# Optimization experiments

Hardware: AMD Instinct MI355X
Metric: run time of the kernel (lower is better)

## Reference

```python
import jax, jax.numpy as jnp
import numpy as np
import math

L, B, D, H = 2048, 4, 1024, 16
DK = D // H
DFF = 4 * D
EPS = 1e-5


def setup_inputs() -> dict:
    key = jax.random.key(0)
    ks = jax.random.split(key, 16)
    s = 1.0 / math.sqrt(D)
    sf = 1.0 / math.sqrt(DFF)
    return {
        "x": jax.random.normal(ks[0], (L, B, D), jnp.float32),
        "Wq": jax.random.normal(ks[1], (D, D), jnp.float32) * s,
        "bq": jnp.zeros((D,), jnp.float32),
        "Wk": jax.random.normal(ks[2], (D, D), jnp.float32) * s,
        "bk": jnp.zeros((D,), jnp.float32),
        "Wv": jax.random.normal(ks[3], (D, D), jnp.float32) * s,
        "bv": jnp.zeros((D,), jnp.float32),
        "Wo": jax.random.normal(ks[4], (D, D), jnp.float32) * s,
        "bo": jnp.zeros((D,), jnp.float32),
        "W1": jax.random.normal(ks[5], (D, DFF), jnp.float32) * s,
        "b1": jnp.zeros((DFF,), jnp.float32),
        "W2": jax.random.normal(ks[6], (DFF, D), jnp.float32) * sf,
        "b2": jnp.zeros((D,), jnp.float32),
        "g1": jnp.ones((D,), jnp.float32),
        "be1": jnp.zeros((D,), jnp.float32),
        "g2": jnp.ones((D,), jnp.float32),
        "be2": jnp.zeros((D,), jnp.float32),
    }


def _layer_norm(x, g, b):
    mu = jnp.mean(x, axis=-1, keepdims=True)
    var = jnp.var(x, axis=-1, keepdims=True)
    return (x - mu) * jax.lax.rsqrt(var + EPS) * g + b


def reference(x, Wq, bq, Wk, bk, Wv, bv, Wo, bo, W1, b1, W2, b2, g1, be1, g2, be2):
    # x: (L, B, D)
    q = x @ Wq + bq
    k = x @ Wk + bk
    v = x @ Wv + bv
    # (L,B,H,dk) -> (B,H,L,dk)
    q = q.reshape(L, B, H, DK).transpose(1, 2, 0, 3)
    k = k.reshape(L, B, H, DK).transpose(1, 2, 0, 3)
    v = v.reshape(L, B, H, DK).transpose(1, 2, 0, 3)
    scale = 1.0 / math.sqrt(DK)
    scores = jnp.einsum('bhqd,bhkd->bhqk', q, k) * scale
    w = jax.nn.softmax(scores, axis=-1)
    attn = jnp.einsum('bhqk,bhkd->bhqd', w, v)  # (B,H,L,dk)
    attn = attn.transpose(2, 0, 1, 3).reshape(L, B, D)
    attn_out = attn @ Wo + bo
    x = _layer_norm(x + attn_out, g1, be1)
    h = jax.nn.gelu(x @ W1 + b1, approximate=False)
    ff = h @ W2 + b2
    return _layer_norm(x + ff, g2, be2)
```

## Files before the change

### kernel.cpp

```cpp
#include <hip/hip_runtime.h>

#define L_   2048
#define B_   4
#define D_   1024
#define H_   16
#define DK_  64
#define DFF_ 4096
#define NT_  (L_*B_)

typedef unsigned short u16;
typedef unsigned int   u32;
typedef __bf16 bf16x8 __attribute__((ext_vector_type(8)));
typedef float  f32x4  __attribute__((ext_vector_type(4)));

__device__ __forceinline__ u16 f2bf(float f) {
  u32 u = __float_as_uint(f);
  u += 0x7fffu + ((u >> 16) & 1u);
  return (u16)(u >> 16);
}
__device__ __forceinline__ float bf2f(u32 lo16) {
  return __uint_as_float(lo16 << 16);
}

#define GLDS16(g, l) __builtin_amdgcn_global_load_lds( \
    (const __attribute__((address_space(1))) void*)(g), \
    (__attribute__((address_space(3))) void*)(l), 16, 0, 0)

#define SCQ_ 0.18033688011112042f

__global__ __launch_bounds__(256) void transpose_w_k(
    const float* __restrict__ W, u16* __restrict__ Wt, int K, int N)
{
  __shared__ float tile[32][33];
  int n0 = blockIdx.x * 32, k0 = blockIdx.y * 32;
  int tx = threadIdx.x, ty = threadIdx.y;
#pragma unroll
  for (int i = ty; i < 32; i += 8)
    tile[i][tx] = W[(size_t)(k0 + i) * N + n0 + tx];
  __syncthreads();
#pragma unroll
  for (int i = ty; i < 32; i += 8)
    Wt[(size_t)(n0 + i) * K + k0 + tx] = f2bf(tile[tx][i]);
}

__global__ __launch_bounds__(256) void transpose_w4_k(
    const float* __restrict__ W0, const float* __restrict__ W1,
    const float* __restrict__ W2, const float* __restrict__ W3,
    u16* __restrict__ dst)
{
  __shared__ float tile[32][33];
  int z = blockIdx.z;
  const float* W = (z == 0) ? W0 : (z == 1) ? W1 : (z == 2) ? W2 : W3;
  u16* Wt = dst + (size_t)z * 1048576;
  int n0 = blockIdx.x * 32, k0 = blockIdx.y * 32;
  int tx = threadIdx.x, ty = threadIdx.y;
#pragma unroll
  for (int i = ty; i < 32; i += 8)
    tile[i][tx] = W[(size_t)(k0 + i) * 1024 + n0 + tx];
  __syncthreads();
#pragma unroll
  for (int i = ty; i < 32; i += 8)
    Wt[(size_t)(n0 + i) * 1024 + k0 + tx] = f2bf(tile[tx][i]);
}

__global__ __launch_bounds__(256) void f32_to_bf16_k(
    const float* __restrict__ in, u16* __restrict__ out, int n4)
{
  int i = blockIdx.x * 256 + threadIdx.x;
  if (i >= n4) return;
  float4 v = ((const float4*)in)[i];
  uint2 r;
  r.x = (u32)f2bf(v.x) | ((u32)f2bf(v.y) << 16);
  r.y = (u32)f2bf(v.z) | ((u32)f2bf(v.w) << 16);
  ((uint2*)out)[i] = r;
}

__global__ __launch_bounds__(256) void bias_concat_k(
    const float* __restrict__ bq, const float* __restrict__ bk,
    const float* __restrict__ bv, float* __restrict__ o)
{
  int i = blockIdx.x * 256 + threadIdx.x;
  float v = (i < 1024) ? bq[i] : ((i < 2048) ? bk[i - 1024] : bv[i - 2048]);
  o[i] = v;
}

template<int EPI>
__global__ __launch_bounds__(512, 2)
void gemm_pipe(const u16* __restrict__ A, const u16* __restrict__ Bt,
               const float* __restrict__ bias, const void* __restrict__ res,
               u16* __restrict__ outb, int M, int N, int K)
{
  constexpr int BM = 256, BN = 128, BK = 64;
  constexpr int ABYTES = BM * BK * 2;
  constexpr int BUFB = (BM + BN) * BK * 2;
  __shared__ char SM[3 * BUFB];

  const int tid = threadIdx.x;
  const int w = tid >> 6, lane = tid & 63;
  const int l15 = lane & 15, l4 = lane >> 4;
  const int NK = K >> 6;

  const int gx = gridDim.x;
  int nwg = gx * gridDim.y;
  int id = blockIdx.y * gx + blockIdx.x;
  int q = nwg >> 3, r = nwg & 7;
  int xcd = id & 7, idx = id >> 3;
  int wg = (xcd < r ? xcd * (q + 1) : r * (q + 1) + (xcd - r) * q) + idx;
  const int m0 = (wg / gx) * BM, n0 = (wg % gx) * BN;
  const int wm = (w >> 1) * 64, wn = (w & 1) * 64;

  const u16* gsrc[6];
#pragma unroll
  for (int u = 0; u < 6; ++u) {
    int o = u * 8192 + tid * 16;
    int row; const u16* base;
    if (o < ABYTES) {
      row = o >> 7;
      base = A + (size_t)(m0 + row) * K;
    } else {
      int ob = o - ABYTES;
      row = ob >> 7;
      base = Bt + (size_t)(n0 + row) * K;
    }
    int col8 = ((o >> 4) & 7) ^ (row & 7);
    gsrc[u] = base + col8 * 8;
  }

  auto stage = [&](int t, int u) {
    const u16* s = gsrc[u] + (size_t)((t < NK) ? t : 0) * BK;
    GLDS16(s, SM + (t % 3) * BUFB + u * 8192 + w * 1024);
  };

  for (int tt = 0; tt < 2; ++tt)
#pragma unroll
    for (int u = 0; u < 6; ++u) stage(tt, u);
  asm volatile("s_waitcnt vmcnt(6)" ::: "memory");
  asm volatile("s_barrier" ::: "memory");

  f32x4 acc[4][4];
#pragma unroll
  for (int i = 0; i < 4; ++i)
#pragma unroll
    for (int j = 0; j < 4; ++j) acc[i][j] = (f32x4){0.f, 0.f, 0.f, 0.f};

  for (int t = 0; t < NK; ++t) {
    const char* rb = SM + (t % 3) * BUFB;
    const int tn = t + 2;
#pragma unroll
    for (int ph = 0; ph < 2; ++ph) {
      bf16x8 af[4], bfr[4];
#pragma unroll
      for (int mi = 0; mi < 4; ++mi) {
        int row = wm + mi * 16 + l15;
        af[mi] = *(const bf16x8*)(rb + row * 128 +
                                  (((ph * 4 + l4) ^ (l15 & 7)) << 4));
      }
      stage(tn, ph * 3 + 0);
#pragma unroll
      for (int nj = 0; nj < 4; ++nj) {
        int row = wn + nj * 16 + l15;
        bfr[nj] = *(const bf16x8*)(rb + ABYTES + row * 128 +
                                   (((ph * 4 + l4) ^ (l15 & 7)) << 4));
      }
      stage(tn, ph * 3 + 1);
      stage(tn, ph * 3 + 2);
      __builtin_amdgcn_s_setprio(1);
#pragma unroll
      for (int mi = 0; mi < 4; ++mi)
#pragma unroll
        for (int nj = 0; nj < 4; ++nj)
          acc[mi][nj] = __builtin_amdgcn_mfma_f32_16x16x32_bf16(
              af[mi], bfr[nj], acc[mi][nj], 0, 0, 0);
      __builtin_amdgcn_s_setprio(0);
    }
    asm volatile("s_waitcnt lgkmcnt(0)" ::: "memory");
    asm volatile("s_waitcnt vmcnt(6)" ::: "memory");
    asm volatile("s_barrier" ::: "memory");
  }
  asm volatile("s_waitcnt vmcnt(0)" ::: "memory");

  const int gm = m0 + wm + l4 * 4;
  const int gn = n0 + wn + l15;
#pragma unroll
  for (int mi = 0; mi < 4; ++mi) {
#pragma unroll
    for (int nj = 0; nj < 4; ++nj) {
      int col = gn + nj * 16;
      float bv = bias[col];
#pragma unroll
      for (int rr = 0; rr < 4; ++rr) {
        int row = gm + mi * 16 + rr;
        float v = acc[mi][nj][rr] + bv;
        if (EPI == 2) {
          float gv = 0.5f * v * (1.f + erff(v * 0.70710678118654752f));
          outb[(size_t)row * N + col] = f2bf(gv);
        } else if (EPI == 3) {
          int which = col >> 10, c1 = col & 1023;
          int ll = row >> 2, bb = row & 3;
          int hh = c1 >> 6, dd = c1 & 63;
          if (which == 0) v *= SCQ_;
          outb[(size_t)which * 8388608 +
               ((((size_t)(bb * H_ + hh)) * L_ + ll) << 6) + dd] = f2bf(v);
        } else if (EPI == 5) {
          size_t idxo = (size_t)row * N + col;
          outb[idxo] = f2bf(v + ((const float*)res)[idxo]);
        } else {
          size_t idxo = (size_t)row * N + col;
          outb[idxo] = f2bf(v + bf2f(((const u16*)res)[idxo]));
        }
      }
    }
  }
}

__global__ __launch_bounds__(256, 3)
void attn_fwd2(const u16* __restrict__ qp, const u16* __restrict__ kp,
               const u16* __restrict__ vp, u16* __restrict__ op)
{
  __shared__ u16 Ks[2][64 * 64];
  __shared__ u16 Vt[2][64 * 64];
  const int tid = threadIdx.x, w = tid >> 6, lane = tid & 63;
  const int l15 = lane & 15, l4 = lane >> 4;
  const int n = blockIdx.x;
  const int bh = (n & 7) | ((n >> 7) << 3);
  const int qi = (n >> 3) & 15;
  const int q0 = qi * 128;
  const u16* qb = qp + (size_t)bh * L_ * DK_;
  const u16* kb = kp + (size_t)bh * L_ * DK_;
  const u16* vb = vp + (size_t)bh * L_ * DK_;

  bf16x8 qf[2][2];
#pragma unroll
  for (int g = 0; g < 2; ++g)
#pragma unroll
    for (int kk = 0; kk < 2; ++kk)
      qf[g][kk] = *(const bf16x8*)&qb[(size_t)(q0 + g * 64 + w * 16 + l15) * DK_ +
                                      kk * 32 + l4 * 8];

  f32x4 accO[2][4];
  f32x4 lacc[2];
#pragma unroll
  for (int g = 0; g < 2; ++g) {
#pragma unroll
    for (int i = 0; i < 4; ++i) accO[g][i] = (f32x4){0.f, 0.f, 0.f, 0.f};
    lacc[g] = (f32x4){0.f, 0.f, 0.f, 0.f};
  }

  bf16x8 oneb;
  {
    u32 ob = (l15 == 0) ? 0x3f803f80u : 0u;
#pragma unroll
    for (int j = 0; j < 4; ++j) ((u32*)&oneb)[j] = ob;
  }

  int rho0 = tid >> 3, rho1 = (256 + tid) >> 3, cseg = lane & 7;
  int kv0 = (rho0 & 32) | ((rho0 & 12) << 1) | ((rho0 & 16) >> 2) | (rho0 & 3);
  int kv1 = (rho1 & 32) | ((rho1 & 12) << 1) | ((rho1 & 16) >> 2) | (rho1 & 3);
  const u16* ksrc0 = kb + (size_t)kv0 * DK_ + ((cseg ^ (rho0 & 7)) << 3);
  const u16* ksrc1 = kb + (size_t)kv1 * DK_ + ((cseg ^ (rho1 & 7)) << 3);

  const int vseg = tid & 7, vkvp = tid >> 3;
  const u16* vsrc = vb + (size_t)(vkvp * 2) * DK_ + vseg * 8;
  u32 voff[8];
#pragma unroll
  for (int dd2 = 0; dd2 < 4; ++dd2) {
    int d0 = vseg * 8 + dd2 * 2, d1 = d0 + 1;
    voff[dd2 * 2] = d0 * 128 +
        ((((vkvp >> 2) ^ (d0 & 7) ^ (d0 >> 3)) << 4) | ((vkvp & 3) << 2));
    voff[dd2 * 2 + 1] = d1 * 128 +
        ((((vkvp >> 2) ^ (d1 & 7) ^ (d1 >> 3)) << 4) | ((vkvp & 3) << 2));
  }

  auto packV = [&](int buf, uint4 a, uint4 b) {
#pragma unroll
    for (int dd2 = 0; dd2 < 4; ++dd2) {
      u32 ai = ((const u32*)&a)[dd2], bi = ((const u32*)&b)[dd2];
      *(u32*)((char*)Vt[buf] + voff[dd2 * 2])     = __builtin_amdgcn_perm(bi, ai, 0x05040100u);
      *(u32*)((char*)Vt[buf] + voff[dd2 * 2 + 1]) = __builtin_amdgcn_perm(bi, ai, 0x07060302u);
    }
  };

  auto exp_pack = [&](f32x4 (&s)[4], u32 (&pk)[2][4]) {
#pragma unroll
    for (int i = 0; i < 4; ++i)
#pragma unroll
      for (int rr = 0; rr < 4; ++rr) s[i][rr] = exp2f(s[i][rr]);
#pragma unroll
    for (int kk = 0; kk < 2; ++kk)
#pragma unroll
      for (int j2 = 0; j2 < 4; ++j2) {
        int nb = kk * 2 + (j2 >> 1);
        int rr = (j2 & 1) * 2;
        u32 rres;
        asm("v_cvt_pk_bf16_f32 %0, %1, %2" : "=v"(rres)
            : "v"(s[nb][rr]), "v"(s[nb][rr + 1]));
        pk[kk][j2] = rres;
      }
  };

  {
    uint4 a = *(const uint4*)vsrc;
    uint4 b = *(const uint4*)(vsrc + DK_);
    GLDS16(ksrc0, &Ks[0][w * 512]);
    GLDS16(ksrc1, &Ks[0][2048 + w * 512]);
    packV(0, a, b);
  }
  __syncthreads();

  constexpr int NTI = L_ / 64;
  for (int t = 0; t < NTI; ++t) {
    const int cur = t & 1;
    const bool pf = (t + 1 < NTI);
    const int tn = pf ? t + 1 : t;

    uint4 va = *(const uint4*)(vsrc + (size_t)(tn * 64) * DK_);
    uint4 vbv = *(const uint4*)(vsrc + (size_t)(tn * 64) * DK_ + DK_);
    if (pf) {
      GLDS16(ksrc0 + (size_t)((t + 1) * 64) * DK_, &Ks[cur ^ 1][w * 512]);
      GLDS16(ksrc1 + (size_t)((t + 1) * 64) * DK_, &Ks[cur ^ 1][2048 + w * 512]);
    }

    f32x4 s0[4], s1[4];
#pragma unroll
    for (int i = 0; i < 4; ++i) {
      s0[i] = (f32x4){0.f, 0.f, 0.f, 0.f};
      s1[i] = (f32x4){0.f, 0.f, 0.f, 0.f};
    }
#pragma unroll
    for (int kk = 0; kk < 2; ++kk) {
#pragma unroll
      for (int nb = 0; nb < 4; ++nb) {
        int row = nb * 16 + l15;
        bf16x8 kf = *(const bf16x8*)((const char*)Ks[cur] + row * 128 +
                                     (((kk * 4 + l4) ^ (row & 7)) << 4));
        s0[nb] = __builtin_amdgcn_mfma_f32_16x16x32_bf16(kf, qf[0][kk], s0[nb], 0, 0, 0);
        s1[nb] = __builtin_amdgcn_mfma_f32_16x16x32_bf16(kf, qf[1][kk], s1[nb], 0, 0, 0);
      }
    }

    u32 pk0[2][4], pk1[2][4];
    exp_pack(s0, pk0);
    exp_pack(s1, pk1);

    if (pf) packV(cur ^ 1, va, vbv);

#pragma unroll
    for (int kk = 0; kk < 2; ++kk) {
      bf16x8 pa0, pa1;
      ((u32*)&pa0)[0] = pk0[kk][0]; ((u32*)&pa0)[1] = pk0[kk][1];
      ((u32*)&pa0)[2] = pk0[kk][2]; ((u32*)&pa0)[3] = pk0[kk][3];
      ((u32*)&pa1)[0] = pk1[kk][0]; ((u32*)&pa1)[1] = pk1[kk][1];
      ((u32*)&pa1)[2] = pk1[kk][2]; ((u32*)&pa1)[3] = pk1[kk][3];
      lacc[0] = __builtin_amdgcn_mfma_f32_16x16x32_bf16(pa0, oneb, lacc[0], 0, 0, 0);
      lacc[1] = __builtin_amdgcn_mfma_f32_16x16x32_bf16(pa1, oneb, lacc[1], 0, 0, 0);
#pragma unroll
      for (int nb2 = 0; nb2 < 4; ++nb2) {
        int drow = nb2 * 16 + l15;
        bf16x8 vf = *(const bf16x8*)((const char*)Vt[cur] + drow * 128 +
                                     (((kk * 4 + l4) ^ (drow & 7) ^ (drow >> 3)) << 4));
        accO[0][nb2] = __builtin_amdgcn_mfma_f32_16x16x32_bf16(pa0, vf, accO[0][nb2], 0, 0, 0);
        accO[1][nb2] = __builtin_amdgcn_mfma_f32_16x16x32_bf16(pa1, vf, accO[1][nb2], 0, 0, 0);
      }
    }
    __syncthreads();
  }

  const int bb = bh >> 4, hh = bh & 15;
#pragma unroll
  for (int g = 0; g < 2; ++g) {
#pragma unroll
    for (int rr = 0; rr < 4; ++rr) {
      float ls = __shfl(lacc[g][rr], l4 << 4);
      float rl = 1.f / ls;
      int qg = q0 + g * 64 + w * 16 + l4 * 4 + rr;
      size_t base = ((size_t)qg * B_ + bb) * D_ + hh * 64;
#pragma unroll
      for (int nb2 = 0; nb2 < 4; ++nb2)
        op[base + nb2 * 16 + l15] = f2bf(accO[g][nb2][rr] * rl);
    }
  }
}

__global__ __launch_bounds__(256) void layernorm_bf_k(
    const u16* __restrict__ y, const float* __restrict__ g, const float* __restrict__ be,
    float* __restrict__ of, u16* __restrict__ ob)
{
  int row = blockIdx.x, tid = threadIdx.x;
  uint2 raw = *(const uint2*)&y[(size_t)row * D_ + tid * 4];
  float v0 = bf2f(raw.x & 0xffffu), v1 = bf2f(raw.x >> 16);
  float v2 = bf2f(raw.y & 0xffffu), v3 = bf2f(raw.y >> 16);
  float s = (v0 + v1) + (v2 + v3);
  float ss = v0 * v0 + v1 * v1 + v2 * v2 + v3 * v3;
#pragma unroll
  for (int msk = 32; msk >= 1; msk >>= 1) {
    s += __shfl_xor(s, msk);
    ss += __shfl_xor(ss, msk);
  }
  __shared__ float rs[4], rss[4];
  if ((tid & 63) == 0) { rs[tid >> 6] = s; rss[tid >> 6] = ss; }
  __syncthreads();
  s = rs[0] + rs[1] + rs[2] + rs[3];
  ss = rss[0] + rss[1] + rss[2] + rss[3];
  float mu = s * (1.f / D_);
  float var = ss * (1.f / D_) - mu * mu;
  float rstd = rsqrtf(var + 1e-5f);
  int c = tid * 4;
  float o0 = (v0 - mu) * rstd * g[c + 0] + be[c + 0];
  float o1 = (v1 - mu) * rstd * g[c + 1] + be[c + 1];
  float o2 = (v2 - mu) * rstd * g[c + 2] + be[c + 2];
  float o3 = (v3 - mu) * rstd * g[c + 3] + be[c + 3];
  if (of) {
    float4 o = {o0, o1, o2, o3};
    *(float4*)&of[(size_t)row * D_ + c] = o;
  }
  if (ob) {
    uint2 r;
    r.x = (u32)f2bf(o0) | ((u32)f2bf(o1) << 16);
    r.y = (u32)f2bf(o2) | ((u32)f2bf(o3) << 16);
    *(uint2*)&ob[(size_t)row * D_ + c] = r;
  }
}

extern "C" void kernel_launch(void* const* d_in, const int* in_sizes, int n_in,
                              void* d_out, int out_size, void* d_ws, size_t ws_size,
                              hipStream_t stream)
{
  const float* x   = (const float*)d_in[0];
  const float* Wq  = (const float*)d_in[1];
  const float* bq  = (const float*)d_in[2];
  const float* Wk  = (const float*)d_in[3];
  const float* bk  = (const float*)d_in[4];
  const float* Wv  = (const float*)d_in[5];
  const float* bv  = (const float*)d_in[6];
  const float* Wo  = (const float*)d_in[7];
  const float* bo  = (const float*)d_in[8];
  const float* W1f = (const float*)d_in[9];
  const float* b1  = (const float*)d_in[10];
  const float* W2f = (const float*)d_in[11];
  const float* b2  = (const float*)d_in[12];
  const float* g1  = (const float*)d_in[13];
  const float* be1 = (const float*)d_in[14];
  const float* g2  = (const float*)d_in[15];
  const float* be2 = (const float*)d_in[16];

  char* ws = (char*)d_ws;
  const size_t MB = 1024 * 1024;
  u16* WqT  = (u16*)(ws + 0 * MB);
  u16* WoT  = (u16*)(ws + 6 * MB);
  u16* W1T  = (u16*)(ws + 8 * MB);
  u16* W2T  = (u16*)(ws + 16 * MB);
  u16* xb   = (u16*)(ws + 24 * MB);
  u16* qp   = (u16*)(ws + 40 * MB);
  u16* astd = (u16*)(ws + 88 * MB);
  u16* yb   = (u16*)(ws + 104 * MB);
  u16* x1b  = (u16*)(ws + 120 * MB);
  u16* hbuf = (u16*)(ws + 136 * MB);
  float* bcat = (float*)(ws + 200 * MB);
  u16* kp = qp + 8388608;
  u16* vp = qp + 16777216;

  dim3 tb(32, 8);
  transpose_w4_k<<<dim3(32, 32, 4), tb, 0, stream>>>(Wq, Wk, Wv, Wo, WqT);
  transpose_w_k<<<dim3(128, 32), tb, 0, stream>>>(W1f, W1T, D_, DFF_);
  transpose_w_k<<<dim3(32, 128), tb, 0, stream>>>(W2f, W2T, DFF_, D_);
  f32_to_bf16_k<<<NT_ * D_ / 4 / 256, 256, 0, stream>>>(x, xb, NT_ * D_ / 4);
  bias_concat_k<<<12, 256, 0, stream>>>(bq, bk, bv, bcat);

  gemm_pipe<3><<<dim3(24, 32), 512, 0, stream>>>(
      xb, WqT, bcat, nullptr, qp, NT_, 3072, D_);

  attn_fwd2<<<1024, 256, 0, stream>>>(qp, kp, vp, astd);

  gemm_pipe<5><<<dim3(8, 32), 512, 0, stream>>>(
      astd, WoT, bo, x, yb, NT_, D_, D_);
  layernorm_bf_k<<<NT_, 256, 0, stream>>>(yb, g1, be1, nullptr, x1b);
  gemm_pipe<2><<<dim3(32, 32), 512, 0, stream>>>(
      x1b, W1T, b1, nullptr, hbuf, NT_, DFF_, D_);
  gemm_pipe<6><<<dim3(8, 32), 512, 0, stream>>>(
      hbuf, W2T, b2, x1b, yb, NT_, D_, DFF_);
  layernorm_bf_k<<<NT_, 256, 0, stream>>>(yb, g2, be2, (float*)d_out, nullptr);
}
```

Baseline: 453.5 us.

## Add 256x256-tile double-buffered GEMM for QKV and FFN1 projections

Introduces a new GEMM kernel with 256x256 output tiles, where each wave computes a 128x64 sub-tile, using two LDS buffers instead of three. It is used for the wide QKV (N=3072) and FFN1 (N=4096) GEMMs. The larger tile raises arithmetic intensity and halves the grid. The prefetch of the next K-tile is spread across four MFMA phases with barriers between them. The trade-offs are more accumulator registers, a shallower prefetch pipeline, extra barriers per K step and fewer workgroups to cover the CUs. The narrower N=1024 GEMMs keep the old kernel with a trimmed epilogue.

```diff
diff --git a/kernel.cpp b/kernel.cpp
--- a/kernel.cpp
+++ b/kernel.cpp
@@ -86,14 +86,15 @@
 
 template<int EPI>
 __global__ __launch_bounds__(512, 2)
-void gemm_pipe(const u16* __restrict__ A, const u16* __restrict__ Bt,
-               const float* __restrict__ bias, const void* __restrict__ res,
-               u16* __restrict__ outb, int M, int N, int K)
-{
-  constexpr int BM = 256, BN = 128, BK = 64;
+void gemm8(const u16* __restrict__ A, const u16* __restrict__ Bt,
+           const float* __restrict__ bias, const void* __restrict__ res,
+           u16* __restrict__ outb, int M, int N, int K)
+{
+  constexpr int BM = 256, BN = 256, BK = 64;
   constexpr int ABYTES = BM * BK * 2;
   constexpr int BUFB = (BM + BN) * BK * 2;
-  __shared__ char SM[3 * BUFB];
+  constexpr int NGL = BUFB / 8192;
+  __shared__ char SM[2 * BUFB];
 
   const int tid = threadIdx.x;
   const int w = tid >> 6, lane = tid & 63;
@@ -107,82 +108,82 @@
   int xcd = id & 7, idx = id >> 3;
   int wg = (xcd < r ? xcd * (q + 1) : r * (q + 1) + (xcd - r) * q) + idx;
   const int m0 = (wg / gx) * BM, n0 = (wg % gx) * BN;
-  const int wm = (w >> 1) * 64, wn = (w & 1) * 64;
-
-  const u16* gsrc[6];
-#pragma unroll
-  for (int u = 0; u < 6; ++u) {
+  const int wm = (w >> 2) * 128, wn = (w & 3) * 64;
+
+  const u16* gsrc[NGL];
+#pragma unroll
+  for (int u = 0; u < NGL; ++u) {
     int o = u * 8192 + tid * 16;
     int row; const u16* base;
-    if (o < ABYTES) {
-      row = o >> 7;
-      base = A + (size_t)(m0 + row) * K;
-    } else {
-      int ob = o - ABYTES;
-      row = ob >> 7;
-      base = Bt + (size_t)(n0 + row) * K;
-    }
+    if (o < ABYTES) { row = o >> 7; base = A + (size_t)(m0 + row) * K; }
+    else { row = (o - ABYTES) >> 7; base = Bt + (size_t)(n0 + row) * K; }
     int col8 = ((o >> 4) & 7) ^ (row & 7);
     gsrc[u] = base + col8 * 8;
   }
 
-  auto stage = [&](int t, int u) {
-    const u16* s = gsrc[u] + (size_t)((t < NK) ? t : 0) * BK;
-    GLDS16(s, SM + (t % 3) * BUFB + u * 8192 + w * 1024);
+  auto stage = [&](int tt, int u, char* dst) {
+    GLDS16(gsrc[u] + (size_t)tt * BK, dst + u * 8192 + w * 1024);
   };
 
-  for (int tt = 0; tt < 2; ++tt)
-#pragma unroll
-    for (int u = 0; u < 6; ++u) stage(tt, u);
-  asm volatile("s_waitcnt vmcnt(6)" ::: "memory");
-  asm volatile("s_barrier" ::: "memory");
-
-  f32x4 acc[4][4];
-#pragma unroll
-  for (int i = 0; i < 4; ++i)
+#pragma unroll
+  for (int u = 0; u < NGL; ++u) stage(0, u, SM);
+  asm volatile("s_waitcnt vmcnt(0)" ::: "memory");
+  __builtin_amdgcn_s_barrier();
+
+  f32x4 acc[8][4];
+#pragma unroll
+  for (int i = 0; i < 8; ++i)
 #pragma unroll
     for (int j = 0; j < 4; ++j) acc[i][j] = (f32x4){0.f, 0.f, 0.f, 0.f};
 
   for (int t = 0; t < NK; ++t) {
-    const char* rb = SM + (t % 3) * BUFB;
-    const int tn = t + 2;
-#pragma unroll
-    for (int ph = 0; ph < 2; ++ph) {
-      bf16x8 af[4], bfr[4];
+    const char* rb = SM + (t & 1) * BUFB;
+    char* wb = SM + ((t + 1) & 1) * BUFB;
+    const int tt = (t + 1 < NK) ? t + 1 : 0;
+    bf16x8 bfr[4];
+#pragma unroll
+    for (int ph = 0; ph < 4; ++ph) {
+      const int kk = ph >> 1, mh = ph & 1;
+      bf16x8 af[4];
 #pragma unroll
       for (int mi = 0; mi < 4; ++mi) {
-        int row = wm + mi * 16 + l15;
+        int row = wm + mh * 64 + mi * 16 + l15;
         af[mi] = *(const bf16x8*)(rb + row * 128 +
-                                  (((ph * 4 + l4) ^ (l15 & 7)) << 4));
-      }
-      stage(tn, ph * 3 + 0);
-#pragma unroll
-      for (int nj = 0; nj < 4; ++nj) {
-        int row = wn + nj * 16 + l15;
-        bfr[nj] = *(const bf16x8*)(rb + ABYTES + row * 128 +
-                                   (((ph * 4 + l4) ^ (l15 & 7)) << 4));
-      }
-      stage(tn, ph * 3 + 1);
-      stage(tn, ph * 3 + 2);
+                                  (((kk * 4 + l4) ^ (row & 7)) << 4));
+      }
+      if (mh == 0) {
+#pragma unroll
+        for (int nj = 0; nj < 4; ++nj) {
+          int row = wn + nj * 16 + l15;
+          bfr[nj] = *(const bf16x8*)(rb + ABYTES + row * 128 +
+                                     (((kk * 4 + l4) ^ (row & 7)) << 4));
+        }
+      }
+      if (ph == 0)      { stage(tt, 0, wb); stage(tt, 1, wb); stage(tt, 2, wb); }
+      else if (ph == 1) { stage(tt, 3, wb); stage(tt, 4, wb); stage(tt, 5, wb); }
+      else if (ph == 2) { stage(tt, 6, wb); stage(tt, 7, wb); }
+      __builtin_amdgcn_s_barrier();
+      asm volatile("s_waitcnt lgkmcnt(0)" ::: "memory");
+      __builtin_amdgcn_sched_barrier(0);
       __builtin_amdgcn_s_setprio(1);
 #pragma unroll
       for (int mi = 0; mi < 4; ++mi)
 #pragma unroll
         for (int nj = 0; nj < 4; ++nj)
-          acc[mi][nj] = __builtin_amdgcn_mfma_f32_16x16x32_bf16(
-              af[mi], bfr[nj], acc[mi][nj], 0, 0, 0);
+          acc[mh * 4 + mi][nj] = __builtin_amdgcn_mfma_f32_16x16x32_bf16(
+              af[mi], bfr[nj], acc[mh * 4 + mi][nj], 0, 0, 0);
       __builtin_amdgcn_s_setprio(0);
-    }
-    asm volatile("s_waitcnt lgkmcnt(0)" ::: "memory");
-    asm volatile("s_waitcnt vmcnt(6)" ::: "memory");
-    asm volatile("s_barrier" ::: "memory");
+      if (ph == 3)
+        asm volatile("s_waitcnt vmcnt(0)" ::: "memory");
+      __builtin_amdgcn_s_barrier();
+    }
   }
   asm volatile("s_waitcnt vmcnt(0)" ::: "memory");
 
   const int gm = m0 + wm + l4 * 4;
   const int gn = n0 + wn + l15;
 #pragma unroll
-  for (int mi = 0; mi < 4; ++mi) {
+  for (int mi = 0; mi < 8; ++mi) {
 #pragma unroll
     for (int nj = 0; nj < 4; ++nj) {
       int col = gn + nj * 16;
@@ -213,6 +214,125 @@
   }
 }
 
+template<int EPI>
+__global__ __launch_bounds__(512, 2)
+void gemm_pipe(const u16* __restrict__ A, const u16* __restrict__ Bt,
+               const float* __restrict__ bias, const void* __restrict__ res,
+               u16* __restrict__ outb, int M, int N, int K)
+{
+  constexpr int BM = 256, BN = 128, BK = 64;
+  constexpr int ABYTES = BM * BK * 2;
+  constexpr int BUFB = (BM + BN) * BK * 2;
+  __shared__ char SM[3 * BUFB];
+
+  const int tid = threadIdx.x;
+  const int w = tid >> 6, lane = tid & 63;
+  const int l15 = lane & 15, l4 = lane >> 4;
+  const int NK = K >> 6;
+
+  const int gx = gridDim.x;
+  int nwg = gx * gridDim.y;
+  int id = blockIdx.y * gx + blockIdx.x;
+  int q = nwg >> 3, r = nwg & 7;
+  int xcd = id & 7, idx = id >> 3;
+  int wg = (xcd < r ? xcd * (q + 1) : r * (q + 1) + (xcd - r) * q) + idx;
+  const int m0 = (wg / gx) * BM, n0 = (wg % gx) * BN;
+  const int wm = (w >> 1) * 64, wn = (w & 1) * 64;
+
+  const u16* gsrc[6];
+#pragma unroll
+  for (int u = 0; u < 6; ++u) {
+    int o = u * 8192 + tid * 16;
+    int row; const u16* base;
+    if (o < ABYTES) {
+      row = o >> 7;
+      base = A + (size_t)(m0 + row) * K;
+    } else {
+      int ob = o - ABYTES;
+      row = ob >> 7;
+      base = Bt + (size_t)(n0 + row) * K;
+    }
+    int col8 = ((o >> 4) & 7) ^ (row & 7);
+    gsrc[u] = base + col8 * 8;
+  }
+
+  auto stage = [&](int t, int u) {
+    const u16* s = gsrc[u] + (size_t)((t < NK) ? t : 0) * BK;
+    GLDS16(s, SM + (t % 3) * BUFB + u * 8192 + w * 1024);
+  };
+
+  for (int tt = 0; tt < 2; ++tt)
+#pragma unroll
+    for (int u = 0; u < 6; ++u) stage(tt, u);
+  asm volatile("s_waitcnt vmcnt(6)" ::: "memory");
+  asm volatile("s_barrier" ::: "memory");
+
+  f32x4 acc[4][4];
+#pragma unroll
+  for (int i = 0; i < 4; ++i)
+#pragma unroll
+    for (int j = 0; j < 4; ++j) acc[i][j] = (f32x4){0.f, 0.f, 0.f, 0.f};
+
+  for (int t = 0; t < NK; ++t) {
+    const char* rb = SM + (t % 3) * BUFB;
+    const int tn = t + 2;
+#pragma unroll
+    for (int ph = 0; ph < 2; ++ph) {
+      bf16x8 af[4], bfr[4];
+#pragma unroll
+      for (int mi = 0; mi < 4; ++mi) {
+        int row = wm + mi * 16 + l15;
+        af[mi] = *(const bf16x8*)(rb + row * 128 +
+                                  (((ph * 4 + l4) ^ (l15 & 7)) << 4));
+      }
+      stage(tn, ph * 3 + 0);
+#pragma unroll
+      for (int nj = 0; nj < 4; ++nj) {
+        int row = wn + nj * 16 + l15;
+        bfr[nj] = *(const bf16x8*)(rb + ABYTES + row * 128 +
+                                   (((ph * 4 + l4) ^ (l15 & 7)) << 4));
+      }
+      stage(tn, ph * 3 + 1);
+      stage(tn, ph * 3 + 2);
+      __builtin_amdgcn_s_setprio(1);
+#pragma unroll
+      for (int mi = 0; mi < 4; ++mi)
+#pragma unroll
+        for (int nj = 0; nj < 4; ++nj)
+          acc[mi][nj] = __builtin_amdgcn_mfma_f32_16x16x32_bf16(
+              af[mi], bfr[nj], acc[mi][nj], 0, 0, 0);
+      __builtin_amdgcn_s_setprio(0);
+    }
+    asm volatile("s_waitcnt lgkmcnt(0)" ::: "memory");
+    asm volatile("s_waitcnt vmcnt(6)" ::: "memory");
+    asm volatile("s_barrier" ::: "memory");
+  }
+  asm volatile("s_waitcnt vmcnt(0)" ::: "memory");
+
+  const int gm = m0 + wm + l4 * 4;
+  const int gn = n0 + wn + l15;
+#pragma unroll
+  for (int mi = 0; mi < 4; ++mi) {
+#pragma unroll
+    for (int nj = 0; nj < 4; ++nj) {
+      int col = gn + nj * 16;
+      float bv = bias[col];
+#pragma unroll
+      for (int rr = 0; rr < 4; ++rr) {
+        int row = gm + mi * 16 + rr;
+        float v = acc[mi][nj][rr] + bv;
+        if (EPI == 5) {
+          size_t idxo = (size_t)row * N + col;
+          outb[idxo] = f2bf(v + ((const float*)res)[idxo]);
+        } else {
+          size_t idxo = (size_t)row * N + col;
+          outb[idxo] = f2bf(v + bf2f(((const u16*)res)[idxo]));
+        }
+      }
+    }
+  }
+}
+
 __global__ __launch_bounds__(256, 3)
 void attn_fwd2(const u16* __restrict__ qp, const u16* __restrict__ kp,
                const u16* __restrict__ vp, u16* __restrict__ op)
@@ -466,7 +586,7 @@
   f32_to_bf16_k<<<NT_ * D_ / 4 / 256, 256, 0, stream>>>(x, xb, NT_ * D_ / 4);
   bias_concat_k<<<12, 256, 0, stream>>>(bq, bk, bv, bcat);
 
-  gemm_pipe<3><<<dim3(24, 32), 512, 0, stream>>>(
+  gemm8<3><<<dim3(12, 32), 512, 0, stream>>>(
       xb, WqT, bcat, nullptr, qp, NT_, 3072, D_);
 
   attn_fwd2<<<1024, 256, 0, stream>>>(qp, kp, vp, astd);
@@ -474,7 +594,7 @@
   gemm_pipe<5><<<dim3(8, 32), 512, 0, stream>>>(
       astd, WoT, bo, x, yb, NT_, D_, D_);
   layernorm_bf_k<<<NT_, 256, 0, stream>>>(yb, g1, be1, nullptr, x1b);
-  gemm_pipe<2><<<dim3(32, 32), 512, 0, stream>>>(
+  gemm8<2><<<dim3(16, 32), 512, 0, stream>>>(
       x1b, W1T, b1, nullptr, hbuf, NT_, DFF_, D_);
   gemm_pipe<6><<<dim3(8, 32), 512, 0, stream>>>(
       hbuf, W2T, b2, x1b, yb, NT_, D_, DFF_);
```

New measurement: 439.7 us (median of 3 runs). -3.0%, faster.
